# Optimization experiments

Hardware: AMD Instinct MI355X
Metric: run time of the kernel (lower is better)

Reference implementation:

```python
import jax, jax.numpy as jnp
import numpy as np

B = 8
A = 1614
TOPN = 6
IOU_THR = 0.25
PAD = 224
OUT = 224

def _make_anchors():
    # 6 anchor shapes on the 14x14 map, 6 on 7x7, 9 on 4x4 -> 1614 total,
    # ordered anchor-type-major then row-major spatial to match the [C,H,W] flatten
    # of the tidy conv outputs (as generate_default_anchor_maps does in NTS-Net).
    specs = [
        (14, 32.0, [(48, 48), (64, 48), (48, 64), (80, 80), (96, 64), (64, 96)]),
        (7, 64.0, [(96, 96), (128, 96), (96, 128), (160, 160), (192, 128), (128, 192)]),
        (4, 112.0, [(192, 192), (256, 192), (192, 256), (288, 288), (320, 256), (256, 320), (352, 352), (384, 320), (320, 384)]),
    ]
    blocks = []
    for fm, stride, sizes in specs:
        c = (np.arange(fm) + 0.5) * stride
        cy, cx = np.meshgrid(c, c, indexing='ij')
        for (h, w) in sizes:
            blocks.append(np.stack([cy - h / 2, cx - w / 2, cy + h / 2, cx + w / 2], -1).reshape(-1, 4))
    a = (np.concatenate(blocks, 0) + PAD).astype(np.int64)  # mimic (edge_anchors+224).astype(int)
    return a.astype(np.float32)  # [1614,4] (y0,x0,y1,x1) in padded-image coords

def _conv(x, w, b, stride, pad):
    y = jax.lax.conv_general_dilated(x, w, (stride, stride), [(pad, pad), (pad, pad)],
                                     dimension_numbers=('NCHW', 'OIHW', 'NCHW'))
    return y + b[None, :, None, None]

def _rpn_scores(rpn, wd1, bd1, wd2, bd2, wd3, bd3, wt1, bt1, wt2, bt2, wt3, bt3):
    b = rpn.shape[0]
    d1 = jax.nn.relu(_conv(rpn, wd1, bd1, 1, 1))   # [B,128,14,14]
    d2 = jax.nn.relu(_conv(d1, wd2, bd2, 2, 1))    # [B,128,7,7]
    d3 = jax.nn.relu(_conv(d2, wd3, bd3, 2, 1))    # [B,128,4,4]
    t1 = _conv(d1, wt1, bt1, 1, 0).reshape(b, -1)  # [B,1176]
    t2 = _conv(d2, wt2, bt2, 1, 0).reshape(b, -1)  # [B,294]
    t3 = _conv(d3, wt3, bt3, 1, 0).reshape(b, -1)  # [B,144]
    return jnp.concatenate([t1, t2, t3], axis=1)   # [B,1614]

def _nms_keep(boxes, scores):
    # Greedy NMS over all A anchors; returns keep mask in ORIGINAL anchor order.
    order = jnp.argsort(-scores)
    b = boxes[order]
    y0, x0, y1, x1 = b[:, 0], b[:, 1], b[:, 2], b[:, 3]
    area = (y1 - y0) * (x1 - x0)
    ih = jnp.clip(jnp.minimum(y1[:, None], y1[None, :]) - jnp.maximum(y0[:, None], y0[None, :]), 0)
    iw = jnp.clip(jnp.minimum(x1[:, None], x1[None, :]) - jnp.maximum(x0[:, None], x0[None, :]), 0)
    inter = ih * iw
    iou = inter / (area[:, None] + area[None, :] - inter)
    idx = jnp.arange(A)
    def body(i, supp):
        row = (iou[i] > IOU_THR) & (idx > i)
        return jnp.where(supp[i], supp, supp | row)
    supp = jax.lax.fori_loop(0, A, body, jnp.zeros((A,), bool))
    return jnp.zeros((A,), bool).at[order].set(~supp)

def _crop_resize(img, box):
    # img [3,Hp,Wp]; box int32 (x0,y0,x1,y1).
    # Equivalent to F.interpolate(img[:, y0:y1, x0:x1], (224,224), 'bilinear', align_corners=True)
    x0, y0, x1, y1 = box[0], box[1], box[2], box[3]
    t = jnp.arange(OUT, dtype=jnp.float32) / (OUT - 1)
    sy = y0.astype(jnp.float32) + t * (y1 - 1 - y0).astype(jnp.float32)
    sx = x0.astype(jnp.float32) + t * (x1 - 1 - x0).astype(jnp.float32)
    y0i = jnp.floor(sy).astype(jnp.int32); x0i = jnp.floor(sx).astype(jnp.int32)
    y1i = jnp.minimum(y0i + 1, y1 - 1);    x1i = jnp.minimum(x0i + 1, x1 - 1)
    wy = (sy - y0i.astype(jnp.float32))[None, :, None]
    wx = (sx - x0i.astype(jnp.float32))[None, None, :]
    g = lambda yi, xi: img[:, yi][:, :, xi]  # gather rows then cols -> [3,224,224]
    top = (1 - wx) * g(y0i, x0i) + wx * g(y0i, x1i)
    bot = (1 - wx) * g(y1i, x0i) + wx * g(y1i, x1i)
    return (1 - wy) * top + wy * bot

def setup_inputs():
    key = jax.random.key(0)
    ks = jax.random.split(key, 16)
    n = jax.random.normal
    return {
        'x': n(ks[0], (B, 3, 448, 448), jnp.float32),
        'rpn_feature': n(ks[1], (B, 2048, 14, 14), jnp.float32),
        'anchors': jnp.asarray(_make_anchors()),
        'wd1': 0.02 * n(ks[2], (128, 2048, 3, 3), jnp.float32), 'bd1': 0.01 * n(ks[3], (128,), jnp.float32),
        'wd2': 0.05 * n(ks[4], (128, 128, 3, 3), jnp.float32),  'bd2': 0.01 * n(ks[5], (128,), jnp.float32),
        'wd3': 0.05 * n(ks[6], (128, 128, 3, 3), jnp.float32),  'bd3': 0.01 * n(ks[7], (128,), jnp.float32),
        'wt1': 0.1 * n(ks[8], (6, 128, 1, 1), jnp.float32),     'bt1': 0.01 * n(ks[9], (6,), jnp.float32),
        'wt2': 0.1 * n(ks[10], (6, 128, 1, 1), jnp.float32),    'bt2': 0.01 * n(ks[11], (6,), jnp.float32),
        'wt3': 0.1 * n(ks[12], (9, 128, 1, 1), jnp.float32),    'bt3': 0.01 * n(ks[13], (9,), jnp.float32),
    }

def reference(x, rpn_feature, anchors, wd1, bd1, wd2, bd2, wd3, bd3, wt1, bt1, wt2, bt2, wt3, bt3):
    scores = _rpn_scores(rpn_feature, wd1, bd1, wd2, bd2, wd3, bd3, wt1, bt1, wt2, bt2, wt3, bt3)
    keep = jax.vmap(lambda s: _nms_keep(anchors, s))(scores)           # [B,A] bool
    masked = jnp.where(keep, scores, -jnp.inf)
    top_prob, top_idx = jax.lax.top_k(masked, TOPN)                    # [B,6]
    tb = anchors[top_idx]                                              # [B,6,4] (y0,x0,y1,x1)
    coords = jnp.stack([tb[..., 1], tb[..., 0], tb[..., 3], tb[..., 2]], -1)  # (x0,y0,x1,y1)
    x_pad = jnp.pad(x, ((0, 0), (0, 0), (PAD, PAD), (PAD, PAD)))       # [B,3,896,896]
    bint = coords.astype(jnp.int32)
    part_imgs = jax.vmap(lambda img, bs: jax.vmap(lambda bb: _crop_resize(img, bb))(bs))(x_pad, bint)  # [B,6,3,224,224]
    return part_imgs, coords, top_prob, top_idx
```

## Files before the change

kernel.cpp:

```cpp
#include <hip/hip_runtime.h>
#include <hip/hip_bf16.h>
#include <math.h>
#include <stdint.h>


#define OFF_COORDS 7225344
#define OFF_PROB   7225536
#define OFF_IDX    7225584
#define NA 1614
#define K1TOT 18432

typedef __attribute__((ext_vector_type(8)))  short  short8;
typedef __attribute__((ext_vector_type(16))) float  floatx16;

__device__ inline void split_bf16(float v, unsigned short& h, unsigned short& l)
{
    __hip_bfloat16 hb = __float2bfloat16(v);
    float hv = __bfloat162float(hb);
    __hip_bfloat16 lb = __float2bfloat16(v - hv);
    h = *reinterpret_cast<unsigned short*>(&hb);
    l = *reinterpret_cast<unsigned short*>(&lb);
}

__global__ __launch_bounds__(256) void k_prep_a(const float* __restrict__ rpn,
                                                __hip_bfloat16* __restrict__ ah,
                                                __hip_bfloat16* __restrict__ al)
{
    __shared__ float tile[64][65];
    const int cib  = blockIdx.x * 64;
    const int posb = blockIdx.y * 64;
    const int b    = blockIdx.z;
    const int t    = threadIdx.x;
#pragma unroll
    for (int it = 0; it < 16; ++it) {
        int idx  = it * 256 + t;
        int cil  = idx >> 6;
        int posl = idx & 63;
        int pos  = posb + posl;
        int py = pos >> 4, px = pos & 15;
        int y = py - 1, x = px - 1;
        float v = 0.0f;
        if ((unsigned)y < 14u && (unsigned)x < 14u)
            v = rpn[((size_t)(b * 2048 + cib + cil) * 14 + y) * 14 + x];
        tile[cil][posl] = v;
    }
    __syncthreads();
#pragma unroll
    for (int it = 0; it < 16; ++it) {
        int idx  = it * 256 + t;
        int posl = idx >> 6;
        int cil  = idx & 63;
        float v = tile[cil][posl];
        unsigned short h, l;
        split_bf16(v, h, l);
        size_t o = (size_t)(b * 256 + posb + posl) * 2048 + cib + cil;
        ((unsigned short*)ah)[o] = h;
        ((unsigned short*)al)[o] = l;
    }
}

__global__ __launch_bounds__(256) void k_prep_b(const float* __restrict__ w,
                                                __hip_bfloat16* __restrict__ bh,
                                                __hip_bfloat16* __restrict__ bl)
{
    __shared__ float tile[9][260];
    const int ci0 = blockIdx.x * 256;
    const int co  = blockIdx.y;
    const int t   = threadIdx.x;
    const float* wc = w + (size_t)co * K1TOT + (size_t)ci0 * 9;
#pragma unroll
    for (int it = 0; it < 9; ++it) {
        int i = it * 256 + t;
        float v = wc[i];
        tile[i % 9][i / 9] = v;
    }
    __syncthreads();
#pragma unroll
    for (int tap = 0; tap < 9; ++tap) {
        float v = tile[tap][t];
        unsigned short h, l;
        split_bf16(v, h, l);
        size_t o = (size_t)co * K1TOT + (size_t)tap * 2048 + ci0 + t;
        ((unsigned short*)bh)[o] = h;
        ((unsigned short*)bl)[o] = l;
    }
}

__global__ __launch_bounds__(128) void k_prep_w23(const float* __restrict__ w2,
                                                  const float* __restrict__ w3,
                                                  __hip_bfloat16* __restrict__ b2h,
                                                  __hip_bfloat16* __restrict__ b2l,
                                                  __hip_bfloat16* __restrict__ b3h,
                                                  __hip_bfloat16* __restrict__ b3l)
{
    const int tap = blockIdx.x;
    const int co  = blockIdx.y;
    const int z   = blockIdx.z;
    const int ci  = threadIdx.x;
    const float* w = z ? w3 : w2;
    __hip_bfloat16* bh = z ? b3h : b2h;
    __hip_bfloat16* bl = z ? b3l : b2l;
    float v = w[((size_t)co * 128 + ci) * 9 + tap];
    unsigned short h, l;
    split_bf16(v, h, l);
    size_t o = (size_t)co * 1152 + tap * 128 + ci;
    ((unsigned short*)bh)[o] = h;
    ((unsigned short*)bl)[o] = l;
}

template<int POSN, int OW, int STR, int CIN, int MTOT, int GX>
__global__ __launch_bounds__(256) void k_conv_mfma(const short* __restrict__ ah,
                                                   const short* __restrict__ al,
                                                   const short* __restrict__ bh,
                                                   const short* __restrict__ bl,
                                                   float* __restrict__ partial,
                                                   int chunk)
{
    constexpr int KTOT = CIN * 9;
    __shared__ short AsH[128][40];
    __shared__ short AsL[128][40];
    __shared__ short BsH[128][40];
    __shared__ short BsL[128][40];

    const int t     = threadIdx.x;
    const int lane  = t & 63;
    const int w     = t >> 6;
    const int wm    = (w & 1) * 64;
    const int wn    = (w >> 1) * 64;
    const int lm    = lane & 31;
    const int half  = lane >> 5;

    const int nb = gridDim.x;
    const int id = blockIdx.x;
    int mb, kc;
    if ((nb % (8 * GX)) == 0) {
        int xcd = id & 7;
        int j   = id >> 3;
        int jq  = j / GX;
        mb = j - jq * GX;
        kc = xcd + 8 * jq;
    } else {
        kc = id / GX;
        mb = id - kc * GX;
    }
    const int mbase = mb * 128;
    const int k0    = kc * chunk;
    const int k1    = (k0 + chunk < KTOT) ? (k0 + chunk) : KTOT;

    int arow[2], apos[2]; bool aval[2];
    const int akc = (t & 3) * 8;
#pragma unroll
    for (int i = 0; i < 2; ++i) {
        int row = ((i * 256 + t) >> 2);
        int m   = mbase + row;
        arow[i] = row;
        aval[i] = (m < MTOT);
        int mm = aval[i] ? m : 0;
        int b  = mm / POSN;
        int p  = mm - b * POSN;
        int y  = p / OW;
        int x  = p - y * OW;
        apos[i] = b * 256 + y * STR * 16 + x * STR;
    }

    floatx16 acc[2][2];
#pragma unroll
    for (int mf = 0; mf < 2; ++mf)
#pragma unroll
        for (int nf = 0; nf < 2; ++nf)
#pragma unroll
            for (int r = 0; r < 16; ++r) acc[mf][nf][r] = 0.0f;

    const short8 zero8 = {0, 0, 0, 0, 0, 0, 0, 0};
    short8 rAh[2], rAl[2], rBh[2], rBl[2];

    auto stage_load = [&](int ks) {
        const int tap = ks / CIN;
        const int ci0 = ks - tap * CIN;
        const int dy  = tap / 3, dx = tap - dy * 3;
#pragma unroll
        for (int i = 0; i < 2; ++i) {
            if (aval[i]) {
                size_t g = (size_t)(apos[i] + dy * 16 + dx) * CIN + ci0 + akc;
                rAh[i] = *(const short8*)(ah + g);
                rAl[i] = *(const short8*)(al + g);
            } else { rAh[i] = zero8; rAl[i] = zero8; }
        }
#pragma unroll
        for (int i = 0; i < 2; ++i) {
            int n = ((i * 256 + t) >> 2);
            size_t g = (size_t)n * KTOT + ks + akc;
            rBh[i] = *(const short8*)(bh + g);
            rBl[i] = *(const short8*)(bl + g);
        }
    };

    if (k0 < k1) stage_load(k0);

    for (int ks = k0; ks < k1; ks += 32) {
#pragma unroll
        for (int i = 0; i < 2; ++i) {
            *(short8*)&AsH[arow[i]][akc] = rAh[i];
            *(short8*)&AsL[arow[i]][akc] = rAl[i];
        }
#pragma unroll
        for (int i = 0; i < 2; ++i) {
            int n = ((i * 256 + t) >> 2);
            *(short8*)&BsH[n][akc] = rBh[i];
            *(short8*)&BsL[n][akc] = rBl[i];
        }
        __syncthreads();
        if (ks + 32 < k1) stage_load(ks + 32);
#pragma unroll
        for (int kst = 0; kst < 2; ++kst) {
            const int koff = kst * 16 + half * 8;
            short8 a_h[2], a_l[2], b_h[2], b_l[2];
#pragma unroll
            for (int mf = 0; mf < 2; ++mf) {
                a_h[mf] = *(const short8*)&AsH[wm + mf * 32 + lm][koff];
                a_l[mf] = *(const short8*)&AsL[wm + mf * 32 + lm][koff];
            }
#pragma unroll
            for (int nf = 0; nf < 2; ++nf) {
                b_h[nf] = *(const short8*)&BsH[wn + nf * 32 + lm][koff];
                b_l[nf] = *(const short8*)&BsL[wn + nf * 32 + lm][koff];
            }
#pragma unroll
            for (int mf = 0; mf < 2; ++mf)
#pragma unroll
                for (int nf = 0; nf < 2; ++nf) {
                    acc[mf][nf] = __builtin_amdgcn_mfma_f32_32x32x16_bf16(
                        a_h[mf], b_h[nf], acc[mf][nf], 0, 0, 0);
                    acc[mf][nf] = __builtin_amdgcn_mfma_f32_32x32x16_bf16(
                        a_h[mf], b_l[nf], acc[mf][nf], 0, 0, 0);
                    acc[mf][nf] = __builtin_amdgcn_mfma_f32_32x32x16_bf16(
                        a_l[mf], b_h[nf], acc[mf][nf], 0, 0, 0);
                }
        }
        __syncthreads();
    }

    float* P = partial + (size_t)kc * MTOT * 128;
#pragma unroll
    for (int mf = 0; mf < 2; ++mf)
#pragma unroll
        for (int nf = 0; nf < 2; ++nf)
#pragma unroll
            for (int r = 0; r < 16; ++r) {
                int row = (r & 3) + 8 * (r >> 2) + 4 * half;
                int m = mbase + wm + mf * 32 + row;
                int n = wn + nf * 32 + lm;
                if (m < MTOT) P[(size_t)m * 128 + n] = acc[mf][nf][r];
            }
}

template<int POSN, int OWV>
__global__ __launch_bounds__(256) void k_reduce_pad(const float* __restrict__ partial,
                                                    const float* __restrict__ bias,
                                                    float* __restrict__ dn,
                                                    __hip_bfloat16* __restrict__ ph,
                                                    __hip_bfloat16* __restrict__ pl,
                                                    int S)
{
    constexpr int MTOT = 8 * POSN;
    int idx = blockIdx.x * 256 + threadIdx.x;
    int b   = idx >> 13;
    int pos = (idx >> 5) & 255;
    int c4  = idx & 31;
    int y = (pos >> 4) - 1;
    int x = (pos & 15) - 1;
    if ((unsigned)y < (unsigned)OWV && (unsigned)x < (unsigned)OWV) {
        int m = b * POSN + y * OWV + x;
        float4 s = ((const float4*)bias)[c4];
        for (int k = 0; k < S; ++k) {
            float4 p = ((const float4*)(partial + (size_t)k * MTOT * 128 + (size_t)m * 128))[c4];
            s.x += p.x; s.y += p.y; s.z += p.z; s.w += p.w;
        }
        s.x = fmaxf(s.x, 0.0f); s.y = fmaxf(s.y, 0.0f);
        s.z = fmaxf(s.z, 0.0f); s.w = fmaxf(s.w, 0.0f);
        ((float4*)dn)[(size_t)m * 32 + c4] = s;
        ushort4 h, l;
        split_bf16(s.x, h.x, l.x);
        split_bf16(s.y, h.y, l.y);
        split_bf16(s.z, h.z, l.z);
        split_bf16(s.w, h.w, l.w);
        ((ushort4*)ph)[idx] = h;
        ((ushort4*)pl)[idx] = l;
    } else {
        ushort4 z = {0, 0, 0, 0};
        ((ushort4*)ph)[idx] = z;
        ((ushort4*)pl)[idx] = z;
    }
}

__global__ __launch_bounds__(256) void k_reduce3(const float* __restrict__ partial,
                                                 const float* __restrict__ bias,
                                                 float* __restrict__ dn, int S)
{
    int idx = blockIdx.x * 256 + threadIdx.x;
    int c4  = idx & 31;
    float4 s = ((const float4*)bias)[c4];
    for (int k = 0; k < S; ++k) {
        float4 p = ((const float4*)(partial + (size_t)k * 128 * 128))[idx];
        s.x += p.x; s.y += p.y; s.z += p.z; s.w += p.w;
    }
    s.x = fmaxf(s.x, 0.0f); s.y = fmaxf(s.y, 0.0f);
    s.z = fmaxf(s.z, 0.0f); s.w = fmaxf(s.w, 0.0f);
    ((float4*)dn)[idx] = s;
}

__global__ __launch_bounds__(256) void k_heads(const float* __restrict__ d1n,
                                               const float* __restrict__ d2n,
                                               const float* __restrict__ d3n,
                                               const float* __restrict__ w1, const float* __restrict__ b1,
                                               const float* __restrict__ w2, const float* __restrict__ b2,
                                               const float* __restrict__ w3, const float* __restrict__ b3,
                                               float* __restrict__ scores)
{
    int idx = blockIdx.x * 256 + threadIdx.x;
    if (idx >= 8 * NA) return;
    int b = idx / NA;
    int e = idx - b * NA;
    const float* d; const float* w; float bias;
    if (e < 1176) {
        int c = e / 196, p = e - c * 196;
        d = d1n + (size_t)(b * 196 + p) * 128; w = w1 + c * 128; bias = b1[c];
    } else if (e < 1470) {
        int e2 = e - 1176; int c = e2 / 49, p = e2 - c * 49;
        d = d2n + (size_t)(b * 49 + p) * 128; w = w2 + c * 128; bias = b2[c];
    } else {
        int e2 = e - 1470; int c = e2 / 16, p = e2 - c * 16;
        d = d3n + (size_t)(b * 16 + p) * 128; w = w3 + c * 128; bias = b3[c];
    }
    float s = bias;
#pragma unroll
    for (int i = 0; i < 32; ++i) {
        float4 dv = ((const float4*)d)[i];
        float4 wv = ((const float4*)w)[i];
        s = fmaf(dv.x, wv.x, s);
        s = fmaf(dv.y, wv.y, s);
        s = fmaf(dv.z, wv.z, s);
        s = fmaf(dv.w, wv.w, s);
    }
    scores[idx] = s;
}

__global__ __launch_bounds__(256) void k_nms_topk(const float* __restrict__ scores,
                                                  const float* __restrict__ anchors,
                                                  float* __restrict__ out,
                                                  int* __restrict__ boxes)
{
    __shared__ float ms[NA];
    __shared__ float ay0[NA], ax0[NA], ay1[NA], ax1[NA];
    __shared__ unsigned char picked[NA];
    __shared__ float rv[4]; __shared__ int ri[4];
    __shared__ float win[5];
    int b = blockIdx.x;
    int t = threadIdx.x;
    for (int i = t; i < NA; i += 256) {
        ms[i] = scores[b * NA + i];
        float4 an = ((const float4*)anchors)[i];
        ay0[i] = an.x; ax0[i] = an.y; ay1[i] = an.z; ax1[i] = an.w;
        picked[i] = 0;
    }
    __syncthreads();
    for (int r = 0; r < 6; ++r) {
        float bv = -INFINITY; int bi = NA;
        for (int i = t; i < NA; i += 256) {
            if (!picked[i]) {
                float v = ms[i];
                if (v > bv || (v == bv && i < bi)) { bv = v; bi = i; }
            }
        }
#pragma unroll
        for (int off = 32; off > 0; off >>= 1) {
            float v2 = __shfl_down(bv, off);
            int   i2 = __shfl_down(bi, off);
            if (v2 > bv || (v2 == bv && i2 < bi)) { bv = v2; bi = i2; }
        }
        if ((t & 63) == 0) { rv[t >> 6] = bv; ri[t >> 6] = bi; }
        __syncthreads();
        if (t == 0) {
            bv = rv[0]; bi = ri[0];
            for (int wv = 1; wv < 4; ++wv)
                if (rv[wv] > bv || (rv[wv] == bv && ri[wv] < bi)) { bv = rv[wv]; bi = ri[wv]; }
            picked[bi] = 1;
            win[0] = ay0[bi]; win[1] = ax0[bi]; win[2] = ay1[bi]; win[3] = ax1[bi]; win[4] = bv;
            int o = b * 6 + r;
            out[OFF_COORDS + o * 4 + 0] = ax0[bi];
            out[OFF_COORDS + o * 4 + 1] = ay0[bi];
            out[OFF_COORDS + o * 4 + 2] = ax1[bi];
            out[OFF_COORDS + o * 4 + 3] = ay1[bi];
            out[OFF_PROB + o] = bv;
            out[OFF_IDX  + o] = (float)bi;
            boxes[o * 4 + 0] = (int)ax0[bi];
            boxes[o * 4 + 1] = (int)ay0[bi];
            boxes[o * 4 + 2] = (int)ax1[bi];
            boxes[o * 4 + 3] = (int)ay1[bi];
        }
        __syncthreads();
        float by0 = win[0], bx0 = win[1], by1 = win[2], bx1 = win[3];
        float barea = (by1 - by0) * (bx1 - bx0);
        for (int i = t; i < NA; i += 256) {
            if (picked[i]) continue;
            float ih = fmaxf(fminf(by1, ay1[i]) - fmaxf(by0, ay0[i]), 0.0f);
            float iw = fmaxf(fminf(bx1, ax1[i]) - fmaxf(bx0, ax0[i]), 0.0f);
            float inter = ih * iw;
            float area  = (ay1[i] - ay0[i]) * (ax1[i] - ax0[i]);
            float iou = inter / (barea + area - inter);
            if (iou > 0.25f) ms[i] = -INFINITY;
        }
        __syncthreads();
    }
}

__global__ __launch_bounds__(256) void k_crop(const float* __restrict__ x,
                                              const int* __restrict__ boxes,
                                              float* __restrict__ out)
{
    int bid = blockIdx.x;
    int i = threadIdx.x;
    if (i >= 224) return;
    int j   = bid % 224;
    int rem = bid / 224;
    int c   = rem % 3;
    int br  = rem / 3;
    int b   = br / 6;
    int4 bx = ((const int4*)boxes)[br];
    float tj = (float)j / 223.0f;
    float sy = (float)bx.y + tj * (float)(bx.w - 1 - bx.y);
    int y0i = (int)floorf(sy);
    int y1i = min(y0i + 1, bx.w - 1);
    float wy = sy - (float)y0i;
    float ti = (float)i / 223.0f;
    float sx = (float)bx.x + ti * (float)(bx.z - 1 - bx.x);
    int x0i = (int)floorf(sx);
    int x1i = min(x0i + 1, bx.z - 1);
    float wx = sx - (float)x0i;
    const float* img = x + ((size_t)b * 3 + c) * 448 * 448;
    auto g = [&](int yy, int xx) -> float {
        yy -= 224; xx -= 224;
        if ((unsigned)yy >= 448u || (unsigned)xx >= 448u) return 0.0f;
        return img[(size_t)yy * 448 + xx];
    };
    float g00 = g(y0i, x0i), g01 = g(y0i, x1i);
    float g10 = g(y1i, x0i), g11 = g(y1i, x1i);
    float top = (1.0f - wx) * g00 + wx * g01;
    float bot = (1.0f - wx) * g10 + wx * g11;
    out[(size_t)bid * 224 + i] = (1.0f - wy) * top + wy * bot;
}

extern "C" void kernel_launch(void* const* d_in, const int* in_sizes, int n_in,
                              void* d_out, int out_size, void* d_ws, size_t ws_size,
                              hipStream_t stream)
{
    (void)in_sizes; (void)n_in; (void)out_size;
    const float* x    = (const float*)d_in[0];
    const float* rpn  = (const float*)d_in[1];
    const float* anch = (const float*)d_in[2];
    const float* wd1  = (const float*)d_in[3];
    const float* bd1  = (const float*)d_in[4];
    const float* wd2  = (const float*)d_in[5];
    const float* bd2  = (const float*)d_in[6];
    const float* wd3  = (const float*)d_in[7];
    const float* bd3  = (const float*)d_in[8];
    const float* hw1  = (const float*)d_in[9];
    const float* hb1  = (const float*)d_in[10];
    const float* hw2  = (const float*)d_in[11];
    const float* hb2  = (const float*)d_in[12];
    const float* hw3  = (const float*)d_in[13];
    const float* hb3  = (const float*)d_in[14];
    float* out = (float*)d_out;

    char* ws = (char*)d_ws;
    size_t off = 0;
    auto alloc = [&](size_t bytes) -> void* {
        void* p = ws + off;
        off = (off + bytes + 255) & ~(size_t)255;
        return p;
    };
    __hip_bfloat16* ahb  = (__hip_bfloat16*)alloc((size_t)8 * 256 * 2048 * 2);
    __hip_bfloat16* alb  = (__hip_bfloat16*)alloc((size_t)8 * 256 * 2048 * 2);
    __hip_bfloat16* b1h  = (__hip_bfloat16*)alloc((size_t)128 * K1TOT * 2);
    __hip_bfloat16* b1l  = (__hip_bfloat16*)alloc((size_t)128 * K1TOT * 2);
    __hip_bfloat16* b2h  = (__hip_bfloat16*)alloc((size_t)128 * 1152 * 2);
    __hip_bfloat16* b2l  = (__hip_bfloat16*)alloc((size_t)128 * 1152 * 2);
    __hip_bfloat16* b3h  = (__hip_bfloat16*)alloc((size_t)128 * 1152 * 2);
    __hip_bfloat16* b3l  = (__hip_bfloat16*)alloc((size_t)128 * 1152 * 2);
    __hip_bfloat16* d1ph = (__hip_bfloat16*)alloc((size_t)8 * 256 * 128 * 2);
    __hip_bfloat16* d1pl = (__hip_bfloat16*)alloc((size_t)8 * 256 * 128 * 2);
    __hip_bfloat16* d2ph = (__hip_bfloat16*)alloc((size_t)8 * 256 * 128 * 2);
    __hip_bfloat16* d2pl = (__hip_bfloat16*)alloc((size_t)8 * 256 * 128 * 2);
    float* d1n  = (float*)alloc((size_t)8 * 196 * 128 * 4);
    float* d2n  = (float*)alloc((size_t)8 * 49 * 128 * 4);
    float* d3n  = (float*)alloc((size_t)8 * 16 * 128 * 4);
    float* sc   = (float*)alloc((size_t)8 * NA * 4);
    int*  boxes = (int*)alloc((size_t)8 * 6 * 4 * 4);
    size_t avail = (ws_size > off) ? (ws_size - off) : 0;
    float* P = (float*)(ws + off);

    long long s1 = (long long)(avail / ((size_t)1568 * 128 * 4));
    if (s1 > 48) s1 = 48;
    if (s1 < 1)  s1 = 1;
    int S1 = (int)s1;
    int chunk1 = ((K1TOT + S1 * 32 - 1) / (S1 * 32)) * 32;

    k_prep_b<<<dim3(8, 128), 256, 0, stream>>>(wd1, b1h, b1l);
    k_prep_w23<<<dim3(9, 128, 2), 128, 0, stream>>>(wd2, wd3, b2h, b2l, b3h, b3l);
    k_prep_a<<<dim3(32, 4, 8), 256, 0, stream>>>(rpn, ahb, alb);

    k_conv_mfma<196, 14, 1, 2048, 1568, 13><<<dim3(13 * S1), 256, 0, stream>>>(
        (const short*)ahb, (const short*)alb, (const short*)b1h, (const short*)b1l, P, chunk1);
    k_reduce_pad<196, 14><<<dim3(256), 256, 0, stream>>>(P, bd1, d1n, d1ph, d1pl, S1);

    k_conv_mfma<49, 7, 2, 128, 392, 4><<<dim3(36), 256, 0, stream>>>(
        (const short*)d1ph, (const short*)d1pl, (const short*)b2h, (const short*)b2l, P, 128);
    k_reduce_pad<49, 7><<<dim3(256), 256, 0, stream>>>(P, bd2, d2n, d2ph, d2pl, 9);

    k_conv_mfma<16, 4, 2, 128, 128, 1><<<dim3(9), 256, 0, stream>>>(
        (const short*)d2ph, (const short*)d2pl, (const short*)b3h, (const short*)b3l, P, 128);
    k_reduce3<<<dim3(16), 256, 0, stream>>>(P, bd3, d3n, 9);

    k_heads<<<dim3((8 * NA + 255) / 256), 256, 0, stream>>>(d1n, d2n, d3n,
        hw1, hb1, hw2, hb2, hw3, hb3, sc);
    k_nms_topk<<<dim3(8), 256, 0, stream>>>(sc, anch, out, boxes);
    k_crop<<<dim3(8 * 6 * 3 * 224), 256, 0, stream>>>(x, boxes, out);
}
```

Baseline: 256.1 us.

## Use direct global-to-LDS loads with double buffering and wider split-K for small convs

The MFMA conv kernel now loads A/B hi/lo tiles straight from global memory into LDS with global_load_lds and double-buffers them. It uses an XOR-swizzled unpadded layout to avoid bank conflicts and drops the register staging and one barrier per step. Out-of-range rows are clamped instead of zero-filled, which is harmless because those rows are never stored. The second and third convs also use a split-K factor derived from workspace size, up to 36, instead of the fixed 9, which raises block counts. The cost is more partial-sum traffic for the reduce kernels.

```diff
diff --git a/kernel.cpp b/kernel.cpp
--- a/kernel.cpp
+++ b/kernel.cpp
@@ -20,6 +20,14 @@
     __hip_bfloat16 lb = __float2bfloat16(v - hv);
     h = *reinterpret_cast<unsigned short*>(&hb);
     l = *reinterpret_cast<unsigned short*>(&lb);
+}
+
+__device__ __forceinline__ void gload_lds16(const short* g, short* l)
+{
+    __builtin_amdgcn_global_load_lds(
+        (const __attribute__((address_space(1))) unsigned int*)g,
+        (__attribute__((address_space(3))) unsigned int*)l,
+        16, 0, 0);
 }
 
 __global__ __launch_bounds__(256) void k_prep_a(const float* __restrict__ rpn,
@@ -117,10 +125,7 @@
                                                    int chunk)
 {
     constexpr int KTOT = CIN * 9;
-    __shared__ short AsH[128][40];
-    __shared__ short AsL[128][40];
-    __shared__ short BsH[128][40];
-    __shared__ short BsL[128][40];
+    __shared__ short Sm[2][4][4096];
 
     const int t     = threadIdx.x;
     const int lane  = t & 63;
@@ -146,22 +151,26 @@
     const int mbase = mb * 128;
     const int k0    = kc * chunk;
     const int k1    = (k0 + chunk < KTOT) ? (k0 + chunk) : KTOT;
-
-    int arow[2], apos[2]; bool aval[2];
-    const int akc = (t & 3) * 8;
-#pragma unroll
-    for (int i = 0; i < 2; ++i) {
-        int row = ((i * 256 + t) >> 2);
+    const int nst   = (k1 > k0) ? ((k1 - k0) >> 5) : 0;
+
+    size_t abase[2]; size_t bbase[2];
+#pragma unroll
+    for (int j = 0; j < 2; ++j) {
+        int q   = w * 128 + j * 64 + lane;
+        int row = q >> 2;
+        int c   = (q & 3) ^ ((row >> 1) & 3);
         int m   = mbase + row;
-        arow[i] = row;
-        aval[i] = (m < MTOT);
-        int mm = aval[i] ? m : 0;
-        int b  = mm / POSN;
-        int p  = mm - b * POSN;
+        if (m > MTOT - 1) m = MTOT - 1;
+        int b  = m / POSN;
+        int p  = m - b * POSN;
         int y  = p / OW;
         int x  = p - y * OW;
-        apos[i] = b * 256 + y * STR * 16 + x * STR;
-    }
+        int apos = b * 256 + y * STR * 16 + x * STR;
+        abase[j] = (size_t)apos * CIN + c * 8;
+        bbase[j] = (size_t)row * KTOT + c * 8;
+    }
+    const int ldsoff0 = (w * 128) * 8;
+    const int ldsoff1 = (w * 128 + 64) * 8;
 
     floatx16 acc[2][2];
 #pragma unroll
@@ -171,59 +180,44 @@
 #pragma unroll
             for (int r = 0; r < 16; ++r) acc[mf][nf][r] = 0.0f;
 
-    const short8 zero8 = {0, 0, 0, 0, 0, 0, 0, 0};
-    short8 rAh[2], rAl[2], rBh[2], rBl[2];
-
-    auto stage_load = [&](int ks) {
+    auto stage = [&](int buf, int ks) {
         const int tap = ks / CIN;
         const int ci0 = ks - tap * CIN;
         const int dy  = tap / 3, dx = tap - dy * 3;
-#pragma unroll
-        for (int i = 0; i < 2; ++i) {
-            if (aval[i]) {
-                size_t g = (size_t)(apos[i] + dy * 16 + dx) * CIN + ci0 + akc;
-                rAh[i] = *(const short8*)(ah + g);
-                rAl[i] = *(const short8*)(al + g);
-            } else { rAh[i] = zero8; rAl[i] = zero8; }
-        }
-#pragma unroll
-        for (int i = 0; i < 2; ++i) {
-            int n = ((i * 256 + t) >> 2);
-            size_t g = (size_t)n * KTOT + ks + akc;
-            rBh[i] = *(const short8*)(bh + g);
-            rBl[i] = *(const short8*)(bl + g);
-        }
+        const size_t aoff = (size_t)(dy * 16 + dx) * CIN + ci0;
+        gload_lds16(ah + abase[0] + aoff, &Sm[buf][0][ldsoff0]);
+        gload_lds16(ah + abase[1] + aoff, &Sm[buf][0][ldsoff1]);
+        gload_lds16(al + abase[0] + aoff, &Sm[buf][1][ldsoff0]);
+        gload_lds16(al + abase[1] + aoff, &Sm[buf][1][ldsoff1]);
+        gload_lds16(bh + bbase[0] + ks,   &Sm[buf][2][ldsoff0]);
+        gload_lds16(bh + bbase[1] + ks,   &Sm[buf][2][ldsoff1]);
+        gload_lds16(bl + bbase[0] + ks,   &Sm[buf][3][ldsoff0]);
+        gload_lds16(bl + bbase[1] + ks,   &Sm[buf][3][ldsoff1]);
     };
 
-    if (k0 < k1) stage_load(k0);
-
-    for (int ks = k0; ks < k1; ks += 32) {
-#pragma unroll
-        for (int i = 0; i < 2; ++i) {
-            *(short8*)&AsH[arow[i]][akc] = rAh[i];
-            *(short8*)&AsL[arow[i]][akc] = rAl[i];
-        }
-#pragma unroll
-        for (int i = 0; i < 2; ++i) {
-            int n = ((i * 256 + t) >> 2);
-            *(short8*)&BsH[n][akc] = rBh[i];
-            *(short8*)&BsL[n][akc] = rBl[i];
-        }
-        __syncthreads();
-        if (ks + 32 < k1) stage_load(ks + 32);
+    if (nst > 0) stage(0, k0);
+    __syncthreads();
+
+    int cur = 0;
+    for (int i = 0; i < nst; ++i) {
+        if (i + 1 < nst) stage(cur ^ 1, k0 + ((i + 1) << 5));
 #pragma unroll
         for (int kst = 0; kst < 2; ++kst) {
-            const int koff = kst * 16 + half * 8;
+            const int c = kst * 2 + half;
             short8 a_h[2], a_l[2], b_h[2], b_l[2];
 #pragma unroll
             for (int mf = 0; mf < 2; ++mf) {
-                a_h[mf] = *(const short8*)&AsH[wm + mf * 32 + lm][koff];
-                a_l[mf] = *(const short8*)&AsL[wm + mf * 32 + lm][koff];
+                int r  = wm + mf * 32 + lm;
+                int ch = r * 4 + (c ^ ((r >> 1) & 3));
+                a_h[mf] = *(const short8*)&Sm[cur][0][ch * 8];
+                a_l[mf] = *(const short8*)&Sm[cur][1][ch * 8];
             }
 #pragma unroll
             for (int nf = 0; nf < 2; ++nf) {
-                b_h[nf] = *(const short8*)&BsH[wn + nf * 32 + lm][koff];
-                b_l[nf] = *(const short8*)&BsL[wn + nf * 32 + lm][koff];
+                int r  = wn + nf * 32 + lm;
+                int ch = r * 4 + (c ^ ((r >> 1) & 3));
+                b_h[nf] = *(const short8*)&Sm[cur][2][ch * 8];
+                b_l[nf] = *(const short8*)&Sm[cur][3][ch * 8];
             }
 #pragma unroll
             for (int mf = 0; mf < 2; ++mf)
@@ -238,6 +232,7 @@
                 }
         }
         __syncthreads();
+        cur ^= 1;
     }
 
     float* P = partial + (size_t)kc * MTOT * 128;
@@ -505,6 +500,18 @@
     int S1 = (int)s1;
     int chunk1 = ((K1TOT + S1 * 32 - 1) / (S1 * 32)) * 32;
 
+    long long s2 = (long long)(avail / ((size_t)392 * 128 * 4));
+    if (s2 > 36) s2 = 36;
+    if (s2 < 1)  s2 = 1;
+    int S2 = (int)s2;
+    int chunk2 = ((1152 + S2 * 32 - 1) / (S2 * 32)) * 32;
+
+    long long s3 = (long long)(avail / ((size_t)128 * 128 * 4));
+    if (s3 > 36) s3 = 36;
+    if (s3 < 1)  s3 = 1;
+    int S3 = (int)s3;
+    int chunk3 = ((1152 + S3 * 32 - 1) / (S3 * 32)) * 32;
+
     k_prep_b<<<dim3(8, 128), 256, 0, stream>>>(wd1, b1h, b1l);
     k_prep_w23<<<dim3(9, 128, 2), 128, 0, stream>>>(wd2, wd3, b2h, b2l, b3h, b3l);
     k_prep_a<<<dim3(32, 4, 8), 256, 0, stream>>>(rpn, ahb, alb);
@@ -513,13 +520,13 @@
         (const short*)ahb, (const short*)alb, (const short*)b1h, (const short*)b1l, P, chunk1);
     k_reduce_pad<196, 14><<<dim3(256), 256, 0, stream>>>(P, bd1, d1n, d1ph, d1pl, S1);
 
-    k_conv_mfma<49, 7, 2, 128, 392, 4><<<dim3(36), 256, 0, stream>>>(
-        (const short*)d1ph, (const short*)d1pl, (const short*)b2h, (const short*)b2l, P, 128);
-    k_reduce_pad<49, 7><<<dim3(256), 256, 0, stream>>>(P, bd2, d2n, d2ph, d2pl, 9);
-
-    k_conv_mfma<16, 4, 2, 128, 128, 1><<<dim3(9), 256, 0, stream>>>(
-        (const short*)d2ph, (const short*)d2pl, (const short*)b3h, (const short*)b3l, P, 128);
-    k_reduce3<<<dim3(16), 256, 0, stream>>>(P, bd3, d3n, 9);
+    k_conv_mfma<49, 7, 2, 128, 392, 4><<<dim3(4 * S2), 256, 0, stream>>>(
+        (const short*)d1ph, (const short*)d1pl, (const short*)b2h, (const short*)b2l, P, chunk2);
+    k_reduce_pad<49, 7><<<dim3(256), 256, 0, stream>>>(P, bd2, d2n, d2ph, d2pl, S2);
+
+    k_conv_mfma<16, 4, 2, 128, 128, 1><<<dim3(S3), 256, 0, stream>>>(
+        (const short*)d2ph, (const short*)d2pl, (const short*)b3h, (const short*)b3l, P, chunk3);
+    k_reduce3<<<dim3(16), 256, 0, stream>>>(P, bd3, d3n, S3);
 
     k_heads<<<dim3((8 * NA + 255) / 256), 256, 0, stream>>>(d1n, d2n, d3n,
         hw1, hb1, hw2, hb2, hw3, hb3, sc);
```

After: 265.3 us. +3.6%, slower.
